# Optimization experiments

Hardware: AMD Instinct MI355X
Metric: run time of the kernel (lower is better)

## Reference

```python
import jax, jax.numpy as jnp
import numpy as np

N, E, Q = 50000, 500000, 100000
IN_DIM, HID, EDGE_DIM, NUM_CLASSES = 128, 128, 16, 2


def _glorot(key, shape):
    fan_in, fan_out = shape
    lim = (6.0 / (fan_in + fan_out)) ** 0.5
    return jax.random.uniform(key, shape, jnp.float32, -lim, lim)


def setup_inputs() -> dict:
    key = jax.random.key(0)
    ks = jax.random.split(key, 12)
    return {
        "node_feature": jax.random.normal(ks[0], (N, IN_DIM), jnp.float32),
        "edge_index": jax.random.randint(ks[1], (2, E), 0, N, jnp.int64),
        "edge_feature": jax.random.normal(ks[2], (E, EDGE_DIM), jnp.float32),
        "edge_label_index": jax.random.randint(ks[3], (2, Q), 0, N, jnp.int64),
        # conv1 params
        "c1_pre_W": _glorot(ks[4], (IN_DIM, IN_DIM)),
        "c1_pre_b": jnp.zeros((IN_DIM,), jnp.float32),
        "c1_msg_W": _glorot(ks[5], (2 * IN_DIM + EDGE_DIM, HID)),
        "c1_msg_b": jnp.zeros((HID,), jnp.float32),
        # conv2 params
        "c2_pre_W": _glorot(ks[6], (HID, HID)),
        "c2_pre_b": jnp.zeros((HID,), jnp.float32),
        "c2_msg_W": _glorot(ks[7], (2 * HID + EDGE_DIM, HID)),
        "c2_msg_b": jnp.zeros((HID,), jnp.float32),
        # link-prediction head
        "lp_W": _glorot(ks[8], (2 * HID, NUM_CLASSES)),
        "lp_b": jnp.zeros((NUM_CLASSES,), jnp.float32),
    }


def _mlp_message_conv(x, edge_index, edge_feature, pre_W, pre_b, msg_W, msg_b):
    # pre_conv: Linear + ReLU
    h = jax.nn.relu(x @ pre_W + pre_b)
    src, dst = edge_index[0], edge_index[1]
    # PyG default flow source_to_target: x_i = target, x_j = source
    x_i = h[dst]  # [E, d]
    x_j = h[src]  # [E, d]
    msg = jnp.concatenate([x_i, x_j, edge_feature], axis=1) @ msg_W + msg_b  # [E, out]
    # aggr='add' onto target nodes
    return jax.ops.segment_sum(msg, dst, num_segments=x.shape[0])


def reference(node_feature, edge_index, edge_feature, edge_label_index,
              c1_pre_W, c1_pre_b, c1_msg_W, c1_msg_b,
              c2_pre_W, c2_pre_b, c2_msg_W, c2_msg_b,
              lp_W, lp_b):
    # eval mode: dropout is identity
    x = jax.nn.relu(_mlp_message_conv(node_feature, edge_index, edge_feature,
                                      c1_pre_W, c1_pre_b, c1_msg_W, c1_msg_b))
    x = _mlp_message_conv(x, edge_index, edge_feature,
                          c2_pre_W, c2_pre_b, c2_msg_W, c2_msg_b)
    nodes_first = x[edge_label_index[0]]   # [Q, hid]
    nodes_second = x[edge_label_index[1]]  # [Q, hid]
    pred = jnp.concatenate([nodes_first, nodes_second], axis=-1) @ lp_W + lp_b
    return pred
```

## Files before the change

### kernel.cpp

```cpp
#include <hip/hip_runtime.h>
#include <cstdint>
#include <cstddef>


typedef __attribute__((ext_vector_type(8))) short short8;
typedef __attribute__((ext_vector_type(4))) float float4v;

__device__ __forceinline__ ushort f2b(float f) {
    uint u = __float_as_uint(f);
    u = u + 0x7fff + ((u >> 16) & 1);
    return (ushort)(u >> 16);
}
__device__ __forceinline__ float b2f(ushort h) {
    return __uint_as_float(((uint)h) << 16);
}
__device__ __forceinline__ uint pack2(float a, float b) {
    return (uint)f2b(a) | ((uint)f2b(b) << 16);
}

__device__ __forceinline__ void gload16(const void* gsrc, void* ldst) {
    __builtin_amdgcn_global_load_lds(
        (const __attribute__((address_space(1))) void*)gsrc,
        (__attribute__((address_space(3))) void*)ldst, 16, 0, 0);
}

#define F_MSG     1
#define F_RELU    2
#define F_DEGBIAS 4
#define F_OUTB    8
#define F_HEAD    32

__launch_bounds__(256, 3)
__global__ void gemm_mfma(const ushort* __restrict__ A, const ushort* __restrict__ B,
                          const ushort* __restrict__ EF,
                          const float* __restrict__ DEG, const ushort* __restrict__ Wt,
                          const float* __restrict__ bias, ushort* __restrict__ outB,
                          ushort* __restrict__ outD,
                          const float* __restrict__ lpW, float* __restrict__ z,
                          int M, int Kp, int flags)
{
    __shared__ ushort xs[128 * 64];
    __shared__ ushort ws[128 * 64];
    const int tid  = threadIdx.x;
    const int lane = tid & 63;
    const int wave = tid >> 6;
    const int row0 = blockIdx.x << 7;

    float4v acc[2][8];
#pragma unroll
    for (int m = 0; m < 2; ++m)
#pragma unroll
        for (int t = 0; t < 8; ++t) acc[m][t] = (float4v){0.f, 0.f, 0.f, 0.f};

    const int ar0   = (wave << 5) + (lane & 15);
    const int bcol  = lane & 15;
    const int cxor  = lane & 7;
    const int koffc = lane >> 4;
    const int sw16  = (((lane & 7) ^ (lane >> 3)) << 4);

    for (int kt = 0; kt < Kp; kt += 64) {
        const int tix = kt >> 6;
        __syncthreads();
#pragma unroll
        for (int i = 0; i < 4; ++i) {
            const int wsoff = (wave << 11) + (i << 9);
            gload16((const char*)Wt + (((size_t)((tix << 13) + wsoff)) << 1) + (lane << 4),
                    &ws[wsoff]);
        }
        {
            const char* srcB; size_t strideB; int toffB;
            if (flags & F_MSG) {
                if (tix < 2)      { srcB = (const char*)A;  strideB = 256; toffB = (tix & 1) << 7; }
                else if (tix < 4) { srcB = (const char*)B;  strideB = 256; toffB = (tix & 1) << 7; }
                else              { srcB = (const char*)EF; strideB = 128; toffB = 0; }
            } else {
                srcB = (const char*)A; strideB = 256; toffB = (tix & 1) << 7;
            }
            const int rb = wave << 5;
#pragma unroll
            for (int i = 0; i < 4; ++i) {
                const int gr = min(row0 + rb + (i << 3) + (lane >> 3), M - 1);
                gload16(srcB + (size_t)gr * strideB + toffB + sw16,
                        &xs[(rb + (i << 3)) << 6]);
            }
        }
        __syncthreads();
#pragma unroll
        for (int sc = 0; sc < 8; sc += 4) {
            const int ra = (sc + koffc) ^ cxor;
            const short8 a0 = *(const short8*)&xs[(ar0 << 6) + (ra << 3)];
            const short8 a1 = *(const short8*)&xs[((ar0 + 16) << 6) + (ra << 3)];
#pragma unroll
            for (int t = 0; t < 8; ++t) {
                const short8 bf = *(const short8*)&ws[(((t << 4) + bcol) << 6) + (ra << 3)];
                acc[0][t] = __builtin_amdgcn_mfma_f32_16x16x32_bf16(a0, bf, acc[0][t], 0, 0, 0);
                acc[1][t] = __builtin_amdgcn_mfma_f32_16x16x32_bf16(a1, bf, acc[1][t], 0, 0, 0);
            }
        }
    }

    float bcv[8];
#pragma unroll
    for (int t = 0; t < 8; ++t) bcv[t] = bias[(t << 4) + bcol];

    if (flags & F_HEAD) {
        const float2* lw = (const float2*)lpW;
        float2 wa[8], wb[8];
#pragma unroll
        for (int t = 0; t < 8; ++t) {
            const int col = (t << 4) + bcol;
            wa[t] = lw[col];
            wb[t] = lw[128 + col];
        }
#pragma unroll
        for (int m = 0; m < 2; ++m) {
            const int rbase = row0 + (wave << 5) + (m << 4) + ((lane >> 4) << 2);
#pragma unroll
            for (int r = 0; r < 4; ++r) {
                const int row = rbase + r;
                const float d = (row < M) ? DEG[row] : 0.f;
                float za0 = 0.f, za1 = 0.f, zb0 = 0.f, zb1 = 0.f;
#pragma unroll
                for (int t = 0; t < 8; ++t) {
                    const float v = acc[m][t][r] + d * bcv[t];
                    za0 += v * wa[t].x; za1 += v * wa[t].y;
                    zb0 += v * wb[t].x; zb1 += v * wb[t].y;
                }
#pragma unroll
                for (int mk = 8; mk > 0; mk >>= 1) {
                    za0 += __shfl_xor(za0, mk);
                    za1 += __shfl_xor(za1, mk);
                    zb0 += __shfl_xor(zb0, mk);
                    zb1 += __shfl_xor(zb1, mk);
                }
                if (bcol == 0 && row < M)
                    *(float4*)&z[(size_t)row * 4] = make_float4(za0, za1, zb0, zb1);
            }
        }
    } else {
#pragma unroll
        for (int m = 0; m < 2; ++m) {
            const int rbase = row0 + (wave << 5) + (m << 4) + ((lane >> 4) << 2);
#pragma unroll
            for (int r = 0; r < 4; ++r) {
                const int row = rbase + r;
                if (row >= M) continue;
                const float d = DEG[row];
#pragma unroll
                for (int t = 0; t < 8; ++t) {
                    const int col = (t << 4) + bcol;
                    float v = acc[m][t][r];
                    v += (flags & F_DEGBIAS) ? d * bcv[t] : bcv[t];
                    if (flags & F_RELU) v = fmaxf(v, 0.f);
                    outB[((size_t)row << 7) + col] = f2b(v);
                    if (outD) outD[((size_t)row << 7) + col] = f2b(v * d);
                }
            }
        }
    }
}

__launch_bounds__(256, 3)
__global__ void gemm_msg_pre(const ushort* __restrict__ HD, const ushort* __restrict__ AGG,
                             const ushort* __restrict__ EFP, const float* __restrict__ DEG,
                             const ushort* __restrict__ Wm, const float* __restrict__ bm,
                             const ushort* __restrict__ Wp, const float* __restrict__ bp,
                             ushort* __restrict__ outH, ushort* __restrict__ outHD, int M)
{
    __shared__ ushort smem[128 * 128 + 128 * 64];
    ushort* x2 = smem;
    ushort* ws = smem + 128 * 128;

    const int tid  = threadIdx.x;
    const int lane = tid & 63;
    const int wave = tid >> 6;
    const int row0 = blockIdx.x << 7;

    float4v acc[2][8];
#pragma unroll
    for (int m = 0; m < 2; ++m)
#pragma unroll
        for (int t = 0; t < 8; ++t) acc[m][t] = (float4v){0.f, 0.f, 0.f, 0.f};

    const int ar0   = (wave << 5) + (lane & 15);
    const int bcol  = lane & 15;
    const int cxor  = lane & 7;
    const int koffc = lane >> 4;
    const int sw16  = (((lane & 7) ^ (lane >> 3)) << 4);

    for (int kt = 0; kt < 320; kt += 64) {
        const int tix = kt >> 6;
        __syncthreads();
#pragma unroll
        for (int i = 0; i < 4; ++i) {
            const int wsoff = (wave << 11) + (i << 9);
            gload16((const char*)Wm + (((size_t)((tix << 13) + wsoff)) << 1) + (lane << 4),
                    &ws[wsoff]);
        }
        {
            const char* srcB; size_t strideB; int toffB;
            if (tix < 2)      { srcB = (const char*)HD;  strideB = 256; toffB = (tix & 1) << 7; }
            else if (tix < 4) { srcB = (const char*)AGG; strideB = 256; toffB = (tix & 1) << 7; }
            else              { srcB = (const char*)EFP; strideB = 128; toffB = 0; }
            const int rb = wave << 5;
#pragma unroll
            for (int i = 0; i < 4; ++i) {
                const int gr = min(row0 + rb + (i << 3) + (lane >> 3), M - 1);
                gload16(srcB + (size_t)gr * strideB + toffB + sw16,
                        &smem[(rb + (i << 3)) << 6]);
            }
        }
        __syncthreads();
#pragma unroll
        for (int sc = 0; sc < 8; sc += 4) {
            const int ra = (sc + koffc) ^ cxor;
            const short8 a0 = *(const short8*)&smem[(ar0 << 6) + (ra << 3)];
            const short8 a1 = *(const short8*)&smem[((ar0 + 16) << 6) + (ra << 3)];
#pragma unroll
            for (int t = 0; t < 8; ++t) {
                const short8 bf = *(const short8*)&ws[(((t << 4) + bcol) << 6) + (ra << 3)];
                acc[0][t] = __builtin_amdgcn_mfma_f32_16x16x32_bf16(a0, bf, acc[0][t], 0, 0, 0);
                acc[1][t] = __builtin_amdgcn_mfma_f32_16x16x32_bf16(a1, bf, acc[1][t], 0, 0, 0);
            }
        }
    }

    float bcv1[8];
#pragma unroll
    for (int t = 0; t < 8; ++t) bcv1[t] = bm[(t << 4) + bcol];

    __syncthreads();
#pragma unroll
    for (int m = 0; m < 2; ++m) {
        const int rl0 = (wave << 5) + (m << 4) + ((lane >> 4) << 2);
#pragma unroll
        for (int r = 0; r < 4; ++r) {
            const int rl  = rl0 + r;
            const int row = row0 + rl;
            const float d = (row < M) ? DEG[row] : 0.f;
#pragma unroll
            for (int t = 0; t < 8; ++t) {
                const int col = (t << 4) + bcol;
                const float v = fmaxf(acc[m][t][r] + d * bcv1[t], 0.f);
                const int ch = col >> 3;
                const int st = (ch & 8) | ((ch ^ rl) & 7);
                x2[(rl << 7) + (st << 3) + (col & 7)] = f2b(v);
            }
        }
    }

#pragma unroll
    for (int m = 0; m < 2; ++m)
#pragma unroll
        for (int t = 0; t < 8; ++t) acc[m][t] = (float4v){0.f, 0.f, 0.f, 0.f};

    for (int kt2 = 0; kt2 < 2; ++kt2) {
        __syncthreads();
#pragma unroll
        for (int i = 0; i < 4; ++i) {
            const int wsoff = (wave << 11) + (i << 9);
            gload16((const char*)Wp + (((size_t)((kt2 << 13) + wsoff)) << 1) + (lane << 4),
                    &ws[wsoff]);
        }
        __syncthreads();
#pragma unroll
        for (int sc = 0; sc < 8; sc += 4) {
            const int ra = (sc + koffc) ^ cxor;
            const short8 a0 = *(const short8*)&x2[(ar0 << 7) + (kt2 << 6) + (ra << 3)];
            const short8 a1 = *(const short8*)&x2[((ar0 + 16) << 7) + (kt2 << 6) + (ra << 3)];
#pragma unroll
            for (int t = 0; t < 8; ++t) {
                const short8 bf = *(const short8*)&ws[(((t << 4) + bcol) << 6) + (ra << 3)];
                acc[0][t] = __builtin_amdgcn_mfma_f32_16x16x32_bf16(a0, bf, acc[0][t], 0, 0, 0);
                acc[1][t] = __builtin_amdgcn_mfma_f32_16x16x32_bf16(a1, bf, acc[1][t], 0, 0, 0);
            }
        }
    }

    float bcv2[8];
#pragma unroll
    for (int t = 0; t < 8; ++t) bcv2[t] = bp[(t << 4) + bcol];
#pragma unroll
    for (int m = 0; m < 2; ++m) {
        const int rbase = row0 + (wave << 5) + (m << 4) + ((lane >> 4) << 2);
#pragma unroll
        for (int r = 0; r < 4; ++r) {
            const int row = rbase + r;
            if (row >= M) continue;
            const float d = DEG[row];
#pragma unroll
            for (int t = 0; t < 8; ++t) {
                const int col = (t << 4) + bcol;
                const float v = fmaxf(acc[m][t][r] + bcv2[t], 0.f);
                outH[((size_t)row << 7) + col]  = f2b(v);
                outHD[((size_t)row << 7) + col] = f2b(v * d);
            }
        }
    }
}

__launch_bounds__(256)
__global__ void prep(const float* __restrict__ nf, ushort* __restrict__ nf_bf,
                     const float* __restrict__ c1pW, const float* __restrict__ c2pW,
                     const float* __restrict__ c1mW, const float* __restrict__ c2mW,
                     ushort* __restrict__ wtp1, ushort* __restrict__ wtp2,
                     ushort* __restrict__ wtm1, ushort* __restrict__ wtm2,
                     ushort* __restrict__ efp, int* __restrict__ counts, int N)
{
    const int gtid = blockIdx.x * 256 + threadIdx.x;
    const int gstr = gridDim.x * 256;
    for (int i = gtid; i < N; i += gstr) counts[i] = 0;
    for (int i = gtid; i < N * 16; i += gstr) {
        const float4 f0 = *(const float4*)&nf[(size_t)i * 8];
        const float4 f1 = *(const float4*)&nf[(size_t)i * 8 + 4];
        uint4 v;
        v.x = pack2(f0.x, f0.y); v.y = pack2(f0.z, f0.w);
        v.z = pack2(f1.x, f1.y); v.w = pack2(f1.z, f1.w);
        ((uint4*)nf_bf)[i] = v;
    }
    for (int i = gtid; i < N * 8; i += gstr)
        ((uint4*)efp)[i] = make_uint4(0, 0, 0, 0);
    for (int idx = gtid; idx < 2 * 128 * 64; idx += gstr) {
        const int s = idx & 63, n = (idx >> 6) & 127, t = idx >> 13;
        const int k = t * 64 + (((s >> 3) ^ (n & 7)) << 3) + (s & 7);
        wtp1[idx] = f2b(c1pW[(size_t)k * 128 + n]);
        wtp2[idx] = f2b(c2pW[(size_t)k * 128 + n]);
    }
    for (int idx = gtid; idx < 5 * 128 * 64; idx += gstr) {
        const int s = idx & 63, n = (idx >> 6) & 127, t = idx >> 13;
        const int k = t * 64 + (((s >> 3) ^ (n & 7)) << 3) + (s & 7);
        wtm1[idx] = (k < 272) ? f2b(c1mW[(size_t)k * 128 + n]) : (ushort)0;
        wtm2[idx] = (k < 272) ? f2b(c2mW[(size_t)k * 128 + n]) : (ushort)0;
    }
}

__launch_bounds__(256)
__global__ void hist_kernel(const int* __restrict__ ei, int* __restrict__ counts, int E)
{
    const int e = blockIdx.x * 256 + threadIdx.x;
    if (e < E) atomicAdd(&counts[ei[E + e]], 1);
}

__launch_bounds__(256)
__global__ void scan_phase1(const int* __restrict__ counts, int* __restrict__ rowstart,
                            int* __restrict__ blocksums, int N)
{
    __shared__ int sdata[256];
    const int t = threadIdx.x;
    const int i = blockIdx.x * 256 + t;
    const int v = (i < N) ? counts[i] : 0;
    sdata[t] = v;
    __syncthreads();
    for (int off = 1; off < 256; off <<= 1) {
        const int add = (t >= off) ? sdata[t - off] : 0;
        __syncthreads();
        sdata[t] += add;
        __syncthreads();
    }
    if (i < N) rowstart[i] = sdata[t] - v;
    if (t == 255) blocksums[blockIdx.x] = sdata[255];
}

__launch_bounds__(256)
__global__ void scan_phase23(const int* __restrict__ counts, const int* __restrict__ bs,
                             int* __restrict__ rowstart, int* __restrict__ cursor,
                             float* __restrict__ degf, int N, int E)
{
    __shared__ int sdata[256];
    const int t = threadIdx.x;
    const int vb = blockIdx.x;
    int part = 0;
    for (int j = t; j < vb; j += 256) part += bs[j];
    sdata[t] = part;
    __syncthreads();
    for (int s = 128; s > 0; s >>= 1) {
        if (t < s) sdata[t] += sdata[t + s];
        __syncthreads();
    }
    const int off = sdata[0];
    const int i = vb * 256 + t;
    if (i < N) {
        const int rs = rowstart[i] + off;
        rowstart[i] = rs;
        cursor[i]   = rs;
        degf[i]     = (float)counts[i];
    }
    if (vb == 0 && t == 0) rowstart[N] = E;
}

__launch_bounds__(256)
__global__ void build_elist(const int* __restrict__ ei, int* __restrict__ cursor,
                            int2* __restrict__ elist, int E)
{
    const int e = blockIdx.x * 256 + threadIdx.x;
    if (e >= E) return;
    const int d = ei[E + e];
    const int pos = atomicAdd(&cursor[d], 1);
    elist[pos] = make_int2(ei[e], e);
}

__launch_bounds__(256)
__global__ void gather(const int2* __restrict__ elist, const int* __restrict__ rowstart,
                       const ushort* __restrict__ h, ushort* __restrict__ agg,
                       const float* __restrict__ ef, ushort* __restrict__ aggef,
                       int N, int doEf)
{
    const int tid = threadIdx.x;
    const int grp = tid >> 4;
    const int l   = tid & 15;
    const int nvb = (N + 15) / 16;
    for (int vb = blockIdx.x; vb < nvb; vb += gridDim.x) {
        const int node = vb * 16 + grp;
        if (node >= N) continue;
        const int beg = rowstart[node];
        const int end = rowstart[node + 1];
        float a0 = 0.f, a1 = 0.f, a2 = 0.f, a3 = 0.f;
        float a4 = 0.f, a5 = 0.f, a6 = 0.f, a7 = 0.f;
        float efacc = 0.f;
        for (int k = beg; k < end; k += 16) {
            const int cnt = min(16, end - k);
            const int2 ep = elist[k + min(l, cnt - 1)];
            for (int j = 0; j < cnt; j += 8) {
                uint4 v[8];
                float efv[8];
#pragma unroll
                for (int jj = 0; jj < 8; ++jj) {
                    const int idx = min(j + jj, cnt - 1);
                    const int s = __shfl(ep.x, idx, 16);
                    v[jj] = *(const uint4*)&h[((size_t)s << 7) + (l << 3)];
                    if (doEf) {
                        const int y = __shfl(ep.y, idx, 16);
                        efv[jj] = ef[((size_t)y << 4) + l];
                    }
                }
#pragma unroll
                for (int jj = 0; jj < 8; ++jj) {
                    if (j + jj >= cnt) {
                        v[jj] = make_uint4(0, 0, 0, 0);
                        efv[jj] = 0.f;
                    }
                    a0 += b2f((ushort)(v[jj].x & 0xffff));
                    a1 += b2f((ushort)(v[jj].x >> 16));
                    a2 += b2f((ushort)(v[jj].y & 0xffff));
                    a3 += b2f((ushort)(v[jj].y >> 16));
                    a4 += b2f((ushort)(v[jj].z & 0xffff));
                    a5 += b2f((ushort)(v[jj].z >> 16));
                    a6 += b2f((ushort)(v[jj].w & 0xffff));
                    a7 += b2f((ushort)(v[jj].w >> 16));
                    if (doEf) efacc += efv[jj];
                }
            }
        }
        uint4 o;
        o.x = pack2(a0, a1);
        o.y = pack2(a2, a3);
        o.z = pack2(a4, a5);
        o.w = pack2(a6, a7);
        *(uint4*)&agg[((size_t)node << 7) + (l << 3)] = o;
        if (doEf) aggef[((size_t)node << 6) + l] = f2b(efacc);
    }
}

__launch_bounds__(256)
__global__ void head_kernel(const float4* __restrict__ z, const int* __restrict__ eli,
                            const float* __restrict__ lpb, float* __restrict__ out, int Q)
{
    const int q = blockIdx.x * 256 + threadIdx.x;
    if (q >= Q) return;
    const int a = eli[q];
    const int b = eli[Q + q];
    const float4 za = z[a];
    const float4 zb = z[b];
    float2 o = make_float2(za.x + zb.z + lpb[0], za.y + zb.w + lpb[1]);
    *(float2*)&out[(size_t)q * 2] = o;
}

extern "C" void kernel_launch(void* const* d_in, const int* in_sizes, int n_in,
                              void* d_out, int out_size, void* d_ws, size_t ws_size,
                              hipStream_t stream)
{
    const float* nf   = (const float*)d_in[0];
    const int*   ei   = (const int*)d_in[1];
    const float* ef   = (const float*)d_in[2];
    const int*   eli  = (const int*)d_in[3];
    const float* c1pW = (const float*)d_in[4];
    const float* c1pb = (const float*)d_in[5];
    const float* c1mW = (const float*)d_in[6];
    const float* c1mb = (const float*)d_in[7];
    const float* c2pW = (const float*)d_in[8];
    const float* c2pb = (const float*)d_in[9];
    const float* c2mW = (const float*)d_in[10];
    const float* c2mb = (const float*)d_in[11];
    const float* lpW  = (const float*)d_in[12];
    const float* lpb  = (const float*)d_in[13];
    float* out = (float*)d_out;

    const int N = in_sizes[0] / 128;
    const int E = in_sizes[1] / 2;
    const int Q = in_sizes[3] / 2;

    float* DEG = (float*)d_ws;
    float* z   = DEG + N;
    int* counts    = (int*)(z + (size_t)N * 4);
    int* rowstart  = counts + N;
    int* cursor    = rowstart + N + 1;
    int* blocksums = cursor + N;
    uintptr_t ep8 = (uintptr_t)(blocksums + 1024);
    ep8 = (ep8 + 7) & ~(uintptr_t)7;
    int2* elist = (int2*)ep8;
    uintptr_t up = (uintptr_t)(elist + E);
    up = (up + 15) & ~(uintptr_t)15;
    ushort* nf_bf  = (ushort*)up;
    ushort* h_bf   = nf_bf  + (size_t)N * 128;
    ushort* agg_bf = h_bf   + (size_t)N * 128;
    ushort* hd_bf  = agg_bf + (size_t)N * 128;
    ushort* efp    = hd_bf  + (size_t)N * 128;
    ushort* wtp1   = efp    + (size_t)N * 64;
    ushort* wtm1   = wtp1 + 2 * 128 * 64;
    ushort* wtp2   = wtm1 + 5 * 128 * 64;
    ushort* wtm2   = wtp2 + 2 * 128 * 64;

    const int gemmGrid = (N + 127) / 128;
    const int eGrid    = (E + 255) / 256;
    const int nGrid    = (N + 255) / 256;
    const int gGrid    = (N + 15) / 16;
    const int headGrid = (Q + 255) / 256;

    prep<<<nGrid, 256, 0, stream>>>(nf, nf_bf, c1pW, c2pW, c1mW, c2mW,
                                    wtp1, wtp2, wtm1, wtm2, efp, counts, N);
    hist_kernel<<<eGrid, 256, 0, stream>>>(ei, counts, E);
    scan_phase1<<<nGrid, 256, 0, stream>>>(counts, rowstart, blocksums, N);
    scan_phase23<<<nGrid, 256, 0, stream>>>(counts, blocksums, rowstart, cursor, DEG, N, E);
    build_elist<<<eGrid, 256, 0, stream>>>(ei, cursor, elist, E);

    gemm_mfma<<<gemmGrid, 256, 0, stream>>>(nf_bf, nullptr, nullptr, DEG, wtp1,
                                            c1pb, h_bf, hd_bf, nullptr, nullptr, N, 128,
                                            F_RELU | F_OUTB);
    gather<<<gGrid, 256, 0, stream>>>(elist, rowstart, h_bf, agg_bf, ef, efp, N, 1);

    gemm_msg_pre<<<gemmGrid, 256, 0, stream>>>(hd_bf, agg_bf, efp, DEG, wtm1, c1mb,
                                               wtp2, c2pb, h_bf, hd_bf, N);

    gather<<<gGrid, 256, 0, stream>>>(elist, rowstart, h_bf, agg_bf, nullptr, nullptr, N, 0);
    gemm_mfma<<<gemmGrid, 256, 0, stream>>>(hd_bf, agg_bf, efp, DEG, wtm2,
                                            c2mb, nullptr, nullptr, lpW, z, N, 320,
                                            F_MSG | F_DEGBIAS | F_HEAD);

    head_kernel<<<headGrid, 256, 0, stream>>>((const float4*)z, eli, lpb, out, Q);
}
```

Before: 286.2 us.

## Split gather into two feature-half passes and use nontemporal loads/stores

The neighbor gather kernel now processes 64 of the 128 feature columns per launch. Eight lanes handle each node instead of sixteen, and two launches per layer cover both halves. The working set of gathered rows is halved, which should raise L2/MALL hit rates on the random source-row reads. Edge-list, edge-feature and output accesses use nontemporal hints so they do not pollute cache. The cost is an extra launch per layer and reading the edge list and rowstart twice.

```diff
diff --git a/kernel.cpp b/kernel.cpp
--- a/kernel.cpp
+++ b/kernel.cpp
@@ -5,6 +5,8 @@
 
 typedef __attribute__((ext_vector_type(8))) short short8;
 typedef __attribute__((ext_vector_type(4))) float float4v;
+typedef __attribute__((ext_vector_type(4))) uint uint4v;
+typedef __attribute__((ext_vector_type(2))) float float2v;
 
 __device__ __forceinline__ ushort f2b(float f) {
     uint u = __float_as_uint(f);
@@ -396,68 +398,75 @@
     if (e >= E) return;
     const int d = ei[E + e];
     const int pos = atomicAdd(&cursor[d], 1);
-    elist[pos] = make_int2(ei[e], e);
+    const unsigned long long rec = (unsigned long long)(uint)ei[e]
+                                 | ((unsigned long long)(uint)e << 32);
+    __builtin_nontemporal_store(rec, (unsigned long long*)&elist[pos]);
 }
 
 __launch_bounds__(256)
 __global__ void gather(const int2* __restrict__ elist, const int* __restrict__ rowstart,
                        const ushort* __restrict__ h, ushort* __restrict__ agg,
                        const float* __restrict__ ef, ushort* __restrict__ aggef,
-                       int N, int doEf)
+                       int N, int doEf, int pass)
 {
     const int tid = threadIdx.x;
-    const int grp = tid >> 4;
-    const int l   = tid & 15;
-    const int nvb = (N + 15) / 16;
+    const int grp = tid >> 3;
+    const int l   = tid & 7;
+    const int co  = pass << 6;
+    const int nvb = (N + 31) / 32;
     for (int vb = blockIdx.x; vb < nvb; vb += gridDim.x) {
-        const int node = vb * 16 + grp;
+        const int node = vb * 32 + grp;
         if (node >= N) continue;
         const int beg = rowstart[node];
         const int end = rowstart[node + 1];
         float a0 = 0.f, a1 = 0.f, a2 = 0.f, a3 = 0.f;
         float a4 = 0.f, a5 = 0.f, a6 = 0.f, a7 = 0.f;
-        float efacc = 0.f;
-        for (int k = beg; k < end; k += 16) {
-            const int cnt = min(16, end - k);
-            const int2 ep = elist[k + min(l, cnt - 1)];
-            for (int j = 0; j < cnt; j += 8) {
-                uint4 v[8];
-                float efv[8];
-#pragma unroll
-                for (int jj = 0; jj < 8; ++jj) {
-                    const int idx = min(j + jj, cnt - 1);
-                    const int s = __shfl(ep.x, idx, 16);
-                    v[jj] = *(const uint4*)&h[((size_t)s << 7) + (l << 3)];
-                    if (doEf) {
-                        const int y = __shfl(ep.y, idx, 16);
-                        efv[jj] = ef[((size_t)y << 4) + l];
-                    }
+        float e0 = 0.f, e1 = 0.f;
+        for (int k = beg; k < end; k += 8) {
+            const int cnt = min(8, end - k);
+            const unsigned long long epll = __builtin_nontemporal_load(
+                (const unsigned long long*)&elist[k + min(l, cnt - 1)]);
+            const int epx = (int)(uint)epll;
+            const int epy = (int)(uint)(epll >> 32);
+            uint4 v[8];
+            float2v efv[8];
+#pragma unroll
+            for (int jj = 0; jj < 8; ++jj) {
+                const int idx = min(jj, cnt - 1);
+                const int s = __shfl(epx, idx, 8);
+                v[jj] = *(const uint4*)&h[((size_t)s << 7) + co + (l << 3)];
+                if (doEf) {
+                    const int y = __shfl(epy, idx, 8);
+                    efv[jj] = __builtin_nontemporal_load(
+                        (const float2v*)&ef[((size_t)y << 4) + (l << 1)]);
                 }
-#pragma unroll
-                for (int jj = 0; jj < 8; ++jj) {
-                    if (j + jj >= cnt) {
-                        v[jj] = make_uint4(0, 0, 0, 0);
-                        efv[jj] = 0.f;
-                    }
-                    a0 += b2f((ushort)(v[jj].x & 0xffff));
-                    a1 += b2f((ushort)(v[jj].x >> 16));
-                    a2 += b2f((ushort)(v[jj].y & 0xffff));
-                    a3 += b2f((ushort)(v[jj].y >> 16));
-                    a4 += b2f((ushort)(v[jj].z & 0xffff));
-                    a5 += b2f((ushort)(v[jj].z >> 16));
-                    a6 += b2f((ushort)(v[jj].w & 0xffff));
-                    a7 += b2f((ushort)(v[jj].w >> 16));
-                    if (doEf) efacc += efv[jj];
+            }
+#pragma unroll
+            for (int jj = 0; jj < 8; ++jj) {
+                if (jj >= cnt) {
+                    v[jj] = make_uint4(0, 0, 0, 0);
+                    if (doEf) { efv[jj].x = 0.f; efv[jj].y = 0.f; }
                 }
-            }
-        }
-        uint4 o;
+                a0 += b2f((ushort)(v[jj].x & 0xffff));
+                a1 += b2f((ushort)(v[jj].x >> 16));
+                a2 += b2f((ushort)(v[jj].y & 0xffff));
+                a3 += b2f((ushort)(v[jj].y >> 16));
+                a4 += b2f((ushort)(v[jj].z & 0xffff));
+                a5 += b2f((ushort)(v[jj].z >> 16));
+                a6 += b2f((ushort)(v[jj].w & 0xffff));
+                a7 += b2f((ushort)(v[jj].w >> 16));
+                if (doEf) { e0 += efv[jj].x; e1 += efv[jj].y; }
+            }
+        }
+        uint4v o;
         o.x = pack2(a0, a1);
         o.y = pack2(a2, a3);
         o.z = pack2(a4, a5);
         o.w = pack2(a6, a7);
-        *(uint4*)&agg[((size_t)node << 7) + (l << 3)] = o;
-        if (doEf) aggef[((size_t)node << 6) + l] = f2b(efacc);
+        __builtin_nontemporal_store(o, (uint4v*)&agg[((size_t)node << 7) + co + (l << 3)]);
+        if (doEf)
+            __builtin_nontemporal_store(pack2(e0, e1),
+                                        &((uint*)&aggef[(size_t)node << 6])[l]);
     }
 }
 
@@ -523,7 +532,7 @@
     const int gemmGrid = (N + 127) / 128;
     const int eGrid    = (E + 255) / 256;
     const int nGrid    = (N + 255) / 256;
-    const int gGrid    = (N + 15) / 16;
+    const int gGrid    = (N + 31) / 32;
     const int headGrid = (Q + 255) / 256;
 
     prep<<<nGrid, 256, 0, stream>>>(nf, nf_bf, c1pW, c2pW, c1mW, c2mW,
@@ -536,12 +545,14 @@
     gemm_mfma<<<gemmGrid, 256, 0, stream>>>(nf_bf, nullptr, nullptr, DEG, wtp1,
                                             c1pb, h_bf, hd_bf, nullptr, nullptr, N, 128,
                                             F_RELU | F_OUTB);
-    gather<<<gGrid, 256, 0, stream>>>(elist, rowstart, h_bf, agg_bf, ef, efp, N, 1);
+    gather<<<gGrid, 256, 0, stream>>>(elist, rowstart, h_bf, agg_bf, ef, efp, N, 1, 0);
+    gather<<<gGrid, 256, 0, stream>>>(elist, rowstart, h_bf, agg_bf, nullptr, nullptr, N, 0, 1);
 
     gemm_msg_pre<<<gemmGrid, 256, 0, stream>>>(hd_bf, agg_bf, efp, DEG, wtm1, c1mb,
                                                wtp2, c2pb, h_bf, hd_bf, N);
 
-    gather<<<gGrid, 256, 0, stream>>>(elist, rowstart, h_bf, agg_bf, nullptr, nullptr, N, 0);
+    gather<<<gGrid, 256, 0, stream>>>(elist, rowstart, h_bf, agg_bf, nullptr, nullptr, N, 0, 0);
+    gather<<<gGrid, 256, 0, stream>>>(elist, rowstart, h_bf, agg_bf, nullptr, nullptr, N, 0, 1);
     gemm_mfma<<<gemmGrid, 256, 0, stream>>>(hd_bf, agg_bf, efp, DEG, wtm2,
                                             c2mb, nullptr, nullptr, lpW, z, N, 320,
                                             F_MSG | F_DEGBIAS | F_HEAD);
```

After: 325.3 us. +13.7%, slower.
